# Kernel optimization log

Hardware: AMD Instinct MI355X
Metric: run time of the kernel (lower is better)

The kernel has to match this reference:

```python
import jax, jax.numpy as jnp
import numpy as np

B, N, D, E = 256, 192, 512, 1024
H = E // 2          # MLP hidden = 512
K = 58              # round(0.3 * 192), hardcoded in the torch forward
EPS_L2 = 1e-8
EPS_BN = 1e-5


def setup_inputs() -> dict:
    key = jax.random.key(0)
    ks = jax.random.split(key, 8)
    s = 0.02
    return {
        "all_patch_embeddings": jax.random.normal(ks[0], (B, N, D), dtype=jnp.float32),
        "attention_map": jax.random.uniform(ks[1], (B, N + 1, N + 1), dtype=jnp.float32),
        # fc: Linear(D, E)
        "W_fc": jax.random.normal(ks[2], (E, D), dtype=jnp.float32) * s,
        "b_fc": jnp.zeros((E,), dtype=jnp.float32),
        # mlp layer 0: Linear(D, H) + BatchNorm1d(H) + ReLU
        "W1": jax.random.normal(ks[3], (H, D), dtype=jnp.float32) * s,
        "b1": jnp.zeros((H,), dtype=jnp.float32),
        "gamma1": jnp.ones((H,), dtype=jnp.float32),
        "beta1": jnp.zeros((H,), dtype=jnp.float32),
        # mlp layer 1: Linear(H, E) (no BN/ReLU applied on last layer)
        "W2": jax.random.normal(ks[4], (E, H), dtype=jnp.float32) * s,
        "b2": jnp.zeros((E,), dtype=jnp.float32),
    }


def reference(all_patch_embeddings, attention_map, W_fc, b_fc, W1, b1, gamma1, beta1, W2, b2):
    # CLS-row attention over the 192 patch tokens: [B, N]
    cls_attn = attention_map[:, 0, 1:]
    # torch.sort(descending)[...,:K] == top-k indices (batched, replaces python loop)
    _, idx = jax.lax.top_k(cls_attn, K)                      # [B, K] int32
    # batched gather replacing the per-sample index_select loop
    sel = jnp.take_along_axis(all_patch_embeddings, idx[:, :, None], axis=1)  # [B, K, D]
    # l2norm over last dim
    norm = jnp.sqrt(jnp.sum(sel * sel, axis=-1, keepdims=True)) + EPS_L2
    base = sel / norm
    # .half() cast in the original (round-trip to fp16 precision)
    base = base.astype(jnp.float16).astype(jnp.float32)
    # fc branch
    feat_fc = jnp.einsum('bkd,ed->bke', base, W_fc) + b_fc    # [B, K, E]
    # mlp branch (num_layers=2): Linear -> BN(train-mode batch stats) -> ReLU -> Linear
    h = jnp.einsum('bkd,hd->bkh', base, W1) + b1              # [B, K, H]
    hf = h.reshape(B * K, H)
    mu = jnp.mean(hf, axis=0)
    var = jnp.var(hf, axis=0)
    hf = (hf - mu) * jax.lax.rsqrt(var + EPS_BN) * gamma1 + beta1
    h = jax.nn.relu(hf).reshape(B, K, H)
    feat_mlp = jnp.einsum('bkh,eh->bke', h, W2) + b2          # [B, K, E]
    feats = feat_mlp + feat_fc
    # maxk_pool1d_var with k=1 and lengths == K reduces to max over token dim
    return jnp.max(feats, axis=1).astype(jnp.float32)         # [B, E]
```

## Files before the change

### kernel.cpp

```cpp
#include <hip/hip_runtime.h>
#include <hip/hip_fp16.h>

#define B_ 256
#define N_ 192
#define D_ 512
#define E_ 1024
#define H_ 512
#define K_ 58
#define M_ (B_*K_)
#define M2_ (B_*64)

typedef _Float16 f16;
typedef unsigned int u32;
typedef _Float16 half8 __attribute__((ext_vector_type(8)));
typedef float floatx4 __attribute__((ext_vector_type(4)));

__device__ inline half8 cvt8(float4 f0, float4 f1) {
  half8 r;
  r[0]=(f16)f0.x; r[1]=(f16)f0.y; r[2]=(f16)f0.z; r[3]=(f16)f0.w;
  r[4]=(f16)f1.x; r[5]=(f16)f1.y; r[6]=(f16)f1.z; r[7]=(f16)f1.w;
  return r;
}

__device__ inline void gl_lds16(const f16* g, f16* l) {
  __builtin_amdgcn_global_load_lds((const __attribute__((address_space(1))) u32*)g,
                                   (__attribute__((address_space(3))) u32*)l, 16, 0, 0);
}

__global__ void setup_kernel(const float* __restrict__ Wfc, const float* __restrict__ W2,
                             const float* __restrict__ W1, const float* __restrict__ attn,
                             const float* __restrict__ emb,
                             f16* __restrict__ Wcat, f16* __restrict__ W1_16,
                             f16* __restrict__ A16, float* __restrict__ csum) {
  __shared__ float sv[N_];
  __shared__ int sidx[K_];
  __shared__ int cnt;
  int blk = blockIdx.x, t = threadIdx.x;
  if (blk < 512) {
    int idx = (blk*256 + t)*8;
    int e = idx >> 10, c = idx & 1023;
    const float* src = (c < 512) ? (Wfc + (size_t)e*512 + c)
                                 : (W2  + (size_t)e*512 + (c-512));
    half8 o = cvt8(((const float4*)src)[0], ((const float4*)src)[1]);
    *(uint4*)(Wcat + idx) = *(uint4*)&o;
  } else if (blk < 640) {
    int idx = ((blk-512)*256 + t)*8;
    const float* src = W1 + idx;
    half8 o = cvt8(((const float4*)src)[0], ((const float4*)src)[1]);
    *(uint4*)(W1_16 + idx) = *(uint4*)&o;
  } else if (blk < 896) {
    int b = blk - 640;
    if (t == 0) cnt = 0;
    if (t < N_) sv[t] = attn[(size_t)b*193*193 + 1 + t];
    __syncthreads();
    if (t < N_) {
      float v = sv[t]; int rank = 0;
      for (int j = 0; j < N_; ++j) {
        float vj = sv[j];
        rank += (vj > v) || (vj == v && j < t);
      }
      if (rank < K_) sidx[atomicAdd(&cnt, 1)] = t;
    }
    __syncthreads();
    int w = t >> 6, lane = t & 63;
    for (int slot = w; slot < 64; slot += 4) {
      f16* dst = A16 + ((size_t)b*64 + slot)*1024 + lane*8;
      if (slot < K_) {
        const float* src = emb + ((size_t)b*N_ + sidx[slot])*D_ + lane*8;
        float4 v0 = ((const float4*)src)[0];
        float4 v1 = ((const float4*)src)[1];
        float s = v0.x*v0.x + v0.y*v0.y + v0.z*v0.z + v0.w*v0.w
                + v1.x*v1.x + v1.y*v1.y + v1.z*v1.z + v1.w*v1.w;
        #pragma unroll
        for (int off = 32; off > 0; off >>= 1) s += __shfl_xor(s, off);
        float inv = 1.0f / (sqrtf(s) + 1e-8f);
        half8 o;
        o[0]=(f16)(v0.x*inv); o[1]=(f16)(v0.y*inv); o[2]=(f16)(v0.z*inv); o[3]=(f16)(v0.w*inv);
        o[4]=(f16)(v1.x*inv); o[5]=(f16)(v1.y*inv); o[6]=(f16)(v1.z*inv); o[7]=(f16)(v1.w*inv);
        *(uint4*)dst = *(uint4*)&o;
      } else {
        uint4 z; z.x=0u; z.y=0u; z.z=0u; z.w=0u;
        *(uint4*)dst = z;
      }
    }
  } else {
    float4 z; z.x=0.f; z.y=0.f; z.z=0.f; z.w=0.f;
    ((float4*)csum)[t] = z;
  }
}

__launch_bounds__(256)
__global__ void gemm1_kernel(const f16* __restrict__ A16, const f16* __restrict__ W1_16,
                             const float* __restrict__ b1, f16* __restrict__ Aout,
                             float* __restrict__ csum, float* __restrict__ css) {
  __shared__ f16 sA0[64*32], sA1[64*32];
  __shared__ f16 sB0[128*32], sB1[128*32];
  __shared__ float sSum[4*128], sSS[4*128];
  int t = threadIdx.x;
  int n0 = blockIdx.x * 128;
  int m0 = blockIdx.y * 64;
  int lane = t & 63, w = t >> 6, lm = lane & 15, quad = lane >> 4;
  int lrow = lane >> 2, lseg = lane & 3;
  floatx4 acc[8] = {};
  const f16* Ab = A16 + (size_t)m0*1024;
  const f16* Bb = W1_16 + (size_t)n0*512;
  for (int k0 = 0; k0 < 512; k0 += 64) {
    gl_lds16(Ab + (size_t)(w*16 + lrow)*1024 + k0      + lseg*8, &sA0[w*16*32]);
    gl_lds16(Ab + (size_t)(w*16 + lrow)*1024 + k0 + 32 + lseg*8, &sA1[w*16*32]);
    gl_lds16(Bb + (size_t)(w*16 + lrow)*512 + k0      + lseg*8, &sB0[w*16*32]);
    gl_lds16(Bb + (size_t)(w*16 + lrow)*512 + k0 + 32 + lseg*8, &sB1[w*16*32]);
    gl_lds16(Bb + (size_t)(64 + w*16 + lrow)*512 + k0      + lseg*8, &sB0[(64 + w*16)*32]);
    gl_lds16(Bb + (size_t)(64 + w*16 + lrow)*512 + k0 + 32 + lseg*8, &sB1[(64 + w*16)*32]);
    __syncthreads();
    half8 a0 = *(const half8*)&sA0[(w*16 + lm)*32 + quad*8];
    half8 a1 = *(const half8*)&sA1[(w*16 + lm)*32 + quad*8];
    #pragma unroll
    for (int ct = 0; ct < 8; ++ct) {
      half8 b0 = *(const half8*)&sB0[(ct*16 + lm)*32 + quad*8];
      acc[ct] = __builtin_amdgcn_mfma_f32_16x16x32_f16(a0, b0, acc[ct], 0, 0, 0);
      half8 b1f = *(const half8*)&sB1[(ct*16 + lm)*32 + quad*8];
      acc[ct] = __builtin_amdgcn_mfma_f32_16x16x32_f16(a1, b1f, acc[ct], 0, 0, 0);
    }
    __syncthreads();
  }
  #pragma unroll
  for (int ct = 0; ct < 8; ++ct) {
    int col = n0 + ct*16 + lm;
    float bias = b1[col];
    float s = 0.f, ss = 0.f;
    int rb = w*16 + quad*4;
    #pragma unroll
    for (int r = 0; r < 4; ++r) {
      float x = acc[ct][r] + bias;
      Aout[(size_t)(m0 + rb + r)*1024 + 512 + col] = (f16)x;
      if (rb + r < K_) { s += x; ss += x*x; }
    }
    s  += __shfl_xor(s, 16);  s  += __shfl_xor(s, 32);
    ss += __shfl_xor(ss, 16); ss += __shfl_xor(ss, 32);
    if (lane < 16) { sSum[w*128 + ct*16 + lm] = s; sSS[w*128 + ct*16 + lm] = ss; }
  }
  __syncthreads();
  if (t < 128) {
    float s  = sSum[t] + sSum[128+t] + sSum[256+t] + sSum[384+t];
    float ss = sSS[t]  + sSS[128+t]  + sSS[256+t]  + sSS[384+t];
    atomicAdd(&csum[n0 + t], s);
    atomicAdd(&css[n0 + t], ss);
  }
}

__global__ void bnrelu_kernel(f16* __restrict__ A16, const float* __restrict__ csum,
                              const float* __restrict__ css, const float* __restrict__ gamma,
                              const float* __restrict__ beta) {
  __shared__ float sSc[H_], sSh[H_];
  int t = threadIdx.x;
  for (int j = t; j < H_; j += 256) {
    float mu  = csum[j] * (1.0f/M_);
    float var = css[j] * (1.0f/M_) - mu*mu;
    float sc  = gamma[j] * rsqrtf(var + 1e-5f);
    sSc[j] = sc;
    sSh[j] = beta[j] - mu*sc;
  }
  __syncthreads();
  int r0 = blockIdx.x * 16;
  #pragma unroll
  for (int i = 0; i < 4; ++i) {
    int seg = t + 256*i;
    int row = r0 + (seg >> 6);
    int c0  = (seg & 63) * 8;
    f16* p = A16 + (size_t)row*1024 + 512 + c0;
    if ((row & 63) >= K_) {
      uint4 z; z.x=0u; z.y=0u; z.z=0u; z.w=0u;
      *(uint4*)p = z;
    } else {
      half8 hv = *(const half8*)p;
      half8 o;
      #pragma unroll
      for (int k = 0; k < 8; ++k)
        o[k] = (f16)fmaxf((float)hv[k]*sSc[c0+k] + sSh[c0+k], 0.0f);
      *(uint4*)p = *(uint4*)&o;
    }
  }
}

__launch_bounds__(256)
__global__ void fused_kernel(const f16* __restrict__ A16, const f16* __restrict__ Wcat,
                             const float* __restrict__ bfc, const float* __restrict__ b2,
                             float* __restrict__ out) {
  __shared__ f16 sA0[64*32], sA1[64*32];
  __shared__ f16 sB0[128*32], sB1[128*32];
  __shared__ float sMax[4*128];
  int t = threadIdx.x;
  int e0 = blockIdx.x * 128;
  int b  = blockIdx.y;
  int lane = t & 63, w = t >> 6, lm = lane & 15, quad = lane >> 4;
  int lrow = lane >> 2, lseg = lane & 3;
  floatx4 acc[8] = {};
  const f16* Ab = A16 + (size_t)b*64*1024;
  const f16* Bb = Wcat + (size_t)e0*1024;
  for (int k0 = 0; k0 < 1024; k0 += 64) {
    gl_lds16(Ab + (size_t)(w*16 + lrow)*1024 + k0      + lseg*8, &sA0[w*16*32]);
    gl_lds16(Ab + (size_t)(w*16 + lrow)*1024 + k0 + 32 + lseg*8, &sA1[w*16*32]);
    gl_lds16(Bb + (size_t)(w*16 + lrow)*1024 + k0      + lseg*8, &sB0[w*16*32]);
    gl_lds16(Bb + (size_t)(w*16 + lrow)*1024 + k0 + 32 + lseg*8, &sB1[w*16*32]);
    gl_lds16(Bb + (size_t)(64 + w*16 + lrow)*1024 + k0      + lseg*8, &sB0[(64 + w*16)*32]);
    gl_lds16(Bb + (size_t)(64 + w*16 + lrow)*1024 + k0 + 32 + lseg*8, &sB1[(64 + w*16)*32]);
    __syncthreads();
    half8 a0 = *(const half8*)&sA0[(w*16 + lm)*32 + quad*8];
    half8 a1 = *(const half8*)&sA1[(w*16 + lm)*32 + quad*8];
    #pragma unroll
    for (int ct = 0; ct < 8; ++ct) {
      half8 b0 = *(const half8*)&sB0[(ct*16 + lm)*32 + quad*8];
      acc[ct] = __builtin_amdgcn_mfma_f32_16x16x32_f16(a0, b0, acc[ct], 0, 0, 0);
      half8 b1f = *(const half8*)&sB1[(ct*16 + lm)*32 + quad*8];
      acc[ct] = __builtin_amdgcn_mfma_f32_16x16x32_f16(a1, b1f, acc[ct], 0, 0, 0);
    }
    __syncthreads();
  }
  #pragma unroll
  for (int ct = 0; ct < 8; ++ct) {
    float mx = -3.0e38f;
    int rb = w*16 + quad*4;
    #pragma unroll
    for (int r = 0; r < 4; ++r)
      if (rb + r < K_) mx = fmaxf(mx, acc[ct][r]);
    mx = fmaxf(mx, __shfl_xor(mx, 16));
    mx = fmaxf(mx, __shfl_xor(mx, 32));
    if (lane < 16) sMax[w*128 + ct*16 + lm] = mx;
  }
  __syncthreads();
  if (t < 128) {
    float mx = fmaxf(fmaxf(sMax[t], sMax[128+t]), fmaxf(sMax[256+t], sMax[384+t]));
    int e = e0 + t;
    out[(size_t)b*E_ + e] = mx + bfc[e] + b2[e];
  }
}

extern "C" void kernel_launch(void* const* d_in, const int* in_sizes, int n_in,
                              void* d_out, int out_size, void* d_ws, size_t ws_size,
                              hipStream_t stream) {
  const float* emb   = (const float*)d_in[0];
  const float* attn  = (const float*)d_in[1];
  const float* Wfc   = (const float*)d_in[2];
  const float* bfc   = (const float*)d_in[3];
  const float* W1    = (const float*)d_in[4];
  const float* b1    = (const float*)d_in[5];
  const float* gamma = (const float*)d_in[6];
  const float* beta  = (const float*)d_in[7];
  const float* W2    = (const float*)d_in[8];
  const float* b2    = (const float*)d_in[9];
  float* out = (float*)d_out;

  char* ws = (char*)d_ws;
  f16*   A16   = (f16*)(ws);
  f16*   Wcat  = (f16*)(ws + 33554432);
  f16*   W1_16 = (f16*)(ws + 35651584);
  float* csum  = (float*)(ws + 36175872);
  float* css   = (float*)(ws + 36177920);

  setup_kernel<<<897, 256, 0, stream>>>(Wfc, W2, W1, attn, emb, Wcat, W1_16, A16, csum);
  gemm1_kernel<<<dim3(H_/128, B_), 256, 0, stream>>>(A16, W1_16, b1, A16, csum, css);
  bnrelu_kernel<<<M2_/16, 256, 0, stream>>>(A16, csum, css, gamma, beta);
  fused_kernel<<<dim3(E_/128, B_), 256, 0, stream>>>(A16, Wcat, bfc, b2, out);
}
```

Measured before the change: 266.8 us.

## Use 128x128 MFMA tiles with 2x2 warp layout and XOR-swizzled LDS staging

Both GEMM kernels move from 64x128 block tiles, where each warp owned a 16x128 strip, to 128x128 tiles where each warp computes a 64x64 sub-tile of 4x4 MFMA accumulators. Each block now covers two samples, and the K step drops to 32. LDS staging uses an XOR swizzle on 8-element chunks to avoid bank conflicts on the fragment reads. The aim is more MFMA work per LDS fragment load and less redundant global traffic for the weights. The cost is more accumulator registers and twice as many barrier iterations per K.

```diff
diff --git a/kernel.cpp b/kernel.cpp
--- a/kernel.cpp
+++ b/kernel.cpp
@@ -25,6 +25,13 @@
 __device__ inline void gl_lds16(const f16* g, f16* l) {
   __builtin_amdgcn_global_load_lds((const __attribute__((address_space(1))) u32*)g,
                                    (__attribute__((address_space(3))) u32*)l, 16, 0, 0);
+}
+
+__device__ inline void stage128(const f16* gbase, int gstride, f16* sT, int w, int lane) {
+  int lrow  = lane >> 2;
+  int chunk = (lane & 3) ^ ((lane >> 3) & 3);
+  gl_lds16(gbase + (size_t)(w*16      + lrow)*gstride + chunk*8, &sT[(w*16)*32]);
+  gl_lds16(gbase + (size_t)(64 + w*16 + lrow)*gstride + chunk*8, &sT[(64 + w*16)*32]);
 }
 
 __global__ void setup_kernel(const float* __restrict__ Wfc, const float* __restrict__ W2,
@@ -93,58 +100,59 @@
 __global__ void gemm1_kernel(const f16* __restrict__ A16, const f16* __restrict__ W1_16,
                              const float* __restrict__ b1, f16* __restrict__ Aout,
                              float* __restrict__ csum, float* __restrict__ css) {
-  __shared__ f16 sA0[64*32], sA1[64*32];
-  __shared__ f16 sB0[128*32], sB1[128*32];
-  __shared__ float sSum[4*128], sSS[4*128];
+  __shared__ f16 sA[128*32];
+  __shared__ f16 sB[128*32];
+  __shared__ float sSum[4][64], sSS[4][64];
   int t = threadIdx.x;
   int n0 = blockIdx.x * 128;
-  int m0 = blockIdx.y * 64;
+  int m0 = blockIdx.y * 128;
   int lane = t & 63, w = t >> 6, lm = lane & 15, quad = lane >> 4;
-  int lrow = lane >> 2, lseg = lane & 3;
-  floatx4 acc[8] = {};
+  int rh = w & 1, ch = w >> 1;
+  floatx4 acc[4][4] = {};
   const f16* Ab = A16 + (size_t)m0*1024;
   const f16* Bb = W1_16 + (size_t)n0*512;
-  for (int k0 = 0; k0 < 512; k0 += 64) {
-    gl_lds16(Ab + (size_t)(w*16 + lrow)*1024 + k0      + lseg*8, &sA0[w*16*32]);
-    gl_lds16(Ab + (size_t)(w*16 + lrow)*1024 + k0 + 32 + lseg*8, &sA1[w*16*32]);
-    gl_lds16(Bb + (size_t)(w*16 + lrow)*512 + k0      + lseg*8, &sB0[w*16*32]);
-    gl_lds16(Bb + (size_t)(w*16 + lrow)*512 + k0 + 32 + lseg*8, &sB1[w*16*32]);
-    gl_lds16(Bb + (size_t)(64 + w*16 + lrow)*512 + k0      + lseg*8, &sB0[(64 + w*16)*32]);
-    gl_lds16(Bb + (size_t)(64 + w*16 + lrow)*512 + k0 + 32 + lseg*8, &sB1[(64 + w*16)*32]);
-    __syncthreads();
-    half8 a0 = *(const half8*)&sA0[(w*16 + lm)*32 + quad*8];
-    half8 a1 = *(const half8*)&sA1[(w*16 + lm)*32 + quad*8];
-    #pragma unroll
-    for (int ct = 0; ct < 8; ++ct) {
-      half8 b0 = *(const half8*)&sB0[(ct*16 + lm)*32 + quad*8];
-      acc[ct] = __builtin_amdgcn_mfma_f32_16x16x32_f16(a0, b0, acc[ct], 0, 0, 0);
-      half8 b1f = *(const half8*)&sB1[(ct*16 + lm)*32 + quad*8];
-      acc[ct] = __builtin_amdgcn_mfma_f32_16x16x32_f16(a1, b1f, acc[ct], 0, 0, 0);
-    }
+  int sw = (quad ^ ((lm >> 1) & 3)) * 8;
+  for (int k0 = 0; k0 < 512; k0 += 32) {
+    stage128(Ab + k0, 1024, sA, w, lane);
+    stage128(Bb + k0, 512,  sB, w, lane);
+    __syncthreads();
+    half8 a[4], bf[4];
+    #pragma unroll
+    for (int i = 0; i < 4; ++i) a[i]  = *(const half8*)&sA[(rh*64 + i*16 + lm)*32 + sw];
+    #pragma unroll
+    for (int j = 0; j < 4; ++j) bf[j] = *(const half8*)&sB[(ch*64 + j*16 + lm)*32 + sw];
+    #pragma unroll
+    for (int i = 0; i < 4; ++i)
+      #pragma unroll
+      for (int j = 0; j < 4; ++j)
+        acc[i][j] = __builtin_amdgcn_mfma_f32_16x16x32_f16(a[i], bf[j], acc[i][j], 0, 0, 0);
     __syncthreads();
   }
   #pragma unroll
-  for (int ct = 0; ct < 8; ++ct) {
-    int col = n0 + ct*16 + lm;
+  for (int j = 0; j < 4; ++j) {
+    int col = n0 + ch*64 + j*16 + lm;
     float bias = b1[col];
     float s = 0.f, ss = 0.f;
-    int rb = w*16 + quad*4;
-    #pragma unroll
-    for (int r = 0; r < 4; ++r) {
-      float x = acc[ct][r] + bias;
-      Aout[(size_t)(m0 + rb + r)*1024 + 512 + col] = (f16)x;
-      if (rb + r < K_) { s += x; ss += x*x; }
+    #pragma unroll
+    for (int i = 0; i < 4; ++i) {
+      int rib = i*16 + quad*4;
+      int row = m0 + rh*64 + rib;
+      #pragma unroll
+      for (int r = 0; r < 4; ++r) {
+        float x = acc[i][j][r] + bias;
+        Aout[(size_t)(row + r)*1024 + 512 + col] = (f16)x;
+        if (rib + r < K_) { s += x; ss += x*x; }
+      }
     }
     s  += __shfl_xor(s, 16);  s  += __shfl_xor(s, 32);
     ss += __shfl_xor(ss, 16); ss += __shfl_xor(ss, 32);
-    if (lane < 16) { sSum[w*128 + ct*16 + lm] = s; sSS[w*128 + ct*16 + lm] = ss; }
+    if (lane < 16) { sSum[w][j*16 + lm] = s; sSS[w][j*16 + lm] = ss; }
   }
   __syncthreads();
   if (t < 128) {
-    float s  = sSum[t] + sSum[128+t] + sSum[256+t] + sSum[384+t];
-    float ss = sSS[t]  + sSS[128+t]  + sSS[256+t]  + sSS[384+t];
-    atomicAdd(&csum[n0 + t], s);
-    atomicAdd(&css[n0 + t], ss);
+    int wp = (t >> 6) * 2, ci = t & 63;
+    atomicAdd(&csum[n0 + t], sSum[wp][ci] + sSum[wp+1][ci]);
+    atomicAdd(&css[n0 + t],  sSS[wp][ci]  + sSS[wp+1][ci]);
   }
 }
 
@@ -186,52 +194,54 @@
 __global__ void fused_kernel(const f16* __restrict__ A16, const f16* __restrict__ Wcat,
                              const float* __restrict__ bfc, const float* __restrict__ b2,
                              float* __restrict__ out) {
-  __shared__ f16 sA0[64*32], sA1[64*32];
-  __shared__ f16 sB0[128*32], sB1[128*32];
-  __shared__ float sMax[4*128];
+  __shared__ f16 sA[128*32];
+  __shared__ f16 sB[128*32];
+  __shared__ float sMax[4][64];
   int t = threadIdx.x;
   int e0 = blockIdx.x * 128;
-  int b  = blockIdx.y;
+  int bm = blockIdx.y;
   int lane = t & 63, w = t >> 6, lm = lane & 15, quad = lane >> 4;
-  int lrow = lane >> 2, lseg = lane & 3;
-  floatx4 acc[8] = {};
-  const f16* Ab = A16 + (size_t)b*64*1024;
+  int rh = w & 1, ch = w >> 1;
+  floatx4 acc[4][4] = {};
+  const f16* Ab = A16 + (size_t)bm*128*1024;
   const f16* Bb = Wcat + (size_t)e0*1024;
-  for (int k0 = 0; k0 < 1024; k0 += 64) {
-    gl_lds16(Ab + (size_t)(w*16 + lrow)*1024 + k0      + lseg*8, &sA0[w*16*32]);
-    gl_lds16(Ab + (size_t)(w*16 + lrow)*1024 + k0 + 32 + lseg*8, &sA1[w*16*32]);
-    gl_lds16(Bb + (size_t)(w*16 + lrow)*1024 + k0      + lseg*8, &sB0[w*16*32]);
-    gl_lds16(Bb + (size_t)(w*16 + lrow)*1024 + k0 + 32 + lseg*8, &sB1[w*16*32]);
-    gl_lds16(Bb + (size_t)(64 + w*16 + lrow)*1024 + k0      + lseg*8, &sB0[(64 + w*16)*32]);
-    gl_lds16(Bb + (size_t)(64 + w*16 + lrow)*1024 + k0 + 32 + lseg*8, &sB1[(64 + w*16)*32]);
-    __syncthreads();
-    half8 a0 = *(const half8*)&sA0[(w*16 + lm)*32 + quad*8];
-    half8 a1 = *(const half8*)&sA1[(w*16 + lm)*32 + quad*8];
-    #pragma unroll
-    for (int ct = 0; ct < 8; ++ct) {
-      half8 b0 = *(const half8*)&sB0[(ct*16 + lm)*32 + quad*8];
-      acc[ct] = __builtin_amdgcn_mfma_f32_16x16x32_f16(a0, b0, acc[ct], 0, 0, 0);
-      half8 b1f = *(const half8*)&sB1[(ct*16 + lm)*32 + quad*8];
-      acc[ct] = __builtin_amdgcn_mfma_f32_16x16x32_f16(a1, b1f, acc[ct], 0, 0, 0);
-    }
+  int sw = (quad ^ ((lm >> 1) & 3)) * 8;
+  for (int k0 = 0; k0 < 1024; k0 += 32) {
+    stage128(Ab + k0, 1024, sA, w, lane);
+    stage128(Bb + k0, 1024, sB, w, lane);
+    __syncthreads();
+    half8 a[4], bf[4];
+    #pragma unroll
+    for (int i = 0; i < 4; ++i) a[i]  = *(const half8*)&sA[(rh*64 + i*16 + lm)*32 + sw];
+    #pragma unroll
+    for (int j = 0; j < 4; ++j) bf[j] = *(const half8*)&sB[(ch*64 + j*16 + lm)*32 + sw];
+    #pragma unroll
+    for (int i = 0; i < 4; ++i)
+      #pragma unroll
+      for (int j = 0; j < 4; ++j)
+        acc[i][j] = __builtin_amdgcn_mfma_f32_16x16x32_f16(a[i], bf[j], acc[i][j], 0, 0, 0);
     __syncthreads();
   }
   #pragma unroll
-  for (int ct = 0; ct < 8; ++ct) {
+  for (int j = 0; j < 4; ++j) {
     float mx = -3.0e38f;
-    int rb = w*16 + quad*4;
-    #pragma unroll
-    for (int r = 0; r < 4; ++r)
-      if (rb + r < K_) mx = fmaxf(mx, acc[ct][r]);
+    #pragma unroll
+    for (int i = 0; i < 4; ++i) {
+      int rib = i*16 + quad*4;
+      #pragma unroll
+      for (int r = 0; r < 4; ++r)
+        if (rib + r < K_) mx = fmaxf(mx, acc[i][j][r]);
+    }
     mx = fmaxf(mx, __shfl_xor(mx, 16));
     mx = fmaxf(mx, __shfl_xor(mx, 32));
-    if (lane < 16) sMax[w*128 + ct*16 + lm] = mx;
+    if (lane < 16) sMax[w][j*16 + lm] = mx;
   }
   __syncthreads();
-  if (t < 128) {
-    float mx = fmaxf(fmaxf(sMax[t], sMax[128+t]), fmaxf(sMax[256+t], sMax[384+t]));
-    int e = e0 + t;
-    out[(size_t)b*E_ + e] = mx + bfc[e] + b2[e];
+  {
+    int bb = t >> 7, c = t & 127;
+    float mx = sMax[(c >> 6)*2 + bb][c & 63];
+    int e = e0 + c;
+    out[((size_t)bm*2 + bb)*E_ + e] = mx + bfc[e] + b2[e];
   }
 }
 
@@ -258,7 +268,7 @@
   float* css   = (float*)(ws + 36177920);
 
   setup_kernel<<<897, 256, 0, stream>>>(Wfc, W2, W1, attn, emb, Wcat, W1_16, A16, csum);
-  gemm1_kernel<<<dim3(H_/128, B_), 256, 0, stream>>>(A16, W1_16, b1, A16, csum, css);
+  gemm1_kernel<<<dim3(H_/128, M2_/128), 256, 0, stream>>>(A16, W1_16, b1, A16, csum, css);
   bnrelu_kernel<<<M2_/16, 256, 0, stream>>>(A16, csum, css, gamma, beta);
-  fused_kernel<<<dim3(E_/128, B_), 256, 0, stream>>>(A16, Wcat, bfc, b2, out);
-}
+  fused_kernel<<<dim3(E_/128, M2_/128), 256, 0, stream>>>(A16, Wcat, bfc, b2, out);
+}
```

Measured after the change: 255.1 us. 4.4% less time.
